# Kernel optimization log

Measured on AMD Instinct MI355X. Metric: run time of the kernel, lower is better.

The kernel has to match this reference:

```python
import jax, jax.numpy as jnp
import numpy as np

K, N, M, D, H = 3, 16384, 4096, 128, 64


def _phi(x, W1, b1, W2, b2, W3, b3):
    # x: [n, D]; weights stacked over kernels: W1 [K,H,D], W2/W3 [K,H,H], b* [K,H]
    h1 = jax.nn.softplus(jnp.einsum('nd,khd->knh', x, W1) + b1[:, None, :])
    h2 = jax.nn.softplus(jnp.einsum('knh,kgh->kng', h1, W2) + b2[:, None, :])
    return jnp.einsum('kng,kfg->knf', h2, W3) + b3[:, None, :]  # [K, n, H]


def setup_inputs() -> dict:
    key = jax.random.key(0)
    ks = jax.random.split(key, 10)
    s = lambda shp, fan: jax.random.normal(ks[0], shp)  # placeholder
    inp = {
        'x': jax.random.normal(ks[0], (N, D), jnp.float32),
        'z': jax.random.normal(ks[1], (M, D), jnp.float32),
        'W1': jax.random.normal(ks[2], (K, H, D), jnp.float32) / np.sqrt(H),
        'b1': jax.random.normal(ks[3], (K, H), jnp.float32) / np.sqrt(H),
        'W2': jax.random.normal(ks[4], (K, H, H), jnp.float32) / np.sqrt(H),
        'b2': jax.random.normal(ks[5], (K, H), jnp.float32) / np.sqrt(H),
        'W3': jax.random.normal(ks[6], (K, H, H), jnp.float32) / np.sqrt(H),
        'b3': jax.random.normal(ks[7], (K, H), jnp.float32) / np.sqrt(H),
        'log_sigma': jnp.array([0.0, 0.5185, 1.0], jnp.float32),
        'kernel_weights': jnp.zeros((K,), jnp.float32),
    }
    return inp


def reference(x, z, W1, b1, W2, b2, W3, b3, log_sigma, kernel_weights):
    fx = _phi(x, W1, b1, W2, b2, W3, b3)  # [K, N, H]
    fz = _phi(z, W1, b1, W2, b2, W3, b3)  # [K, M, H]
    # pairwise squared distance via expansion (same math as ((fx-fz)**2).sum(-1))
    sq = (jnp.sum(fx * fx, -1)[:, :, None]
          + jnp.sum(fz * fz, -1)[:, None, :]
          - 2.0 * jnp.einsum('knh,kmh->knm', fx, fz))  # [K, N, M]
    sq = jnp.maximum(sq, 0.0)
    inv2sig = 1.0 / (2.0 * jnp.power(10.0, log_sigma))  # [K]
    kxz = jnp.exp(-inv2sig[:, None, None] * sq)  # [K, N, M]
    w = jax.nn.softmax(kernel_weights)  # [K]
    return jnp.einsum('k,knm->nm', w, kxz)  # [N, M]
```

## Files before the change

### kernel.cpp

```cpp
#include <hip/hip_runtime.h>

typedef _Float16 half8 __attribute__((ext_vector_type(8)));
typedef float floatx4 __attribute__((ext_vector_type(4)));

#define K_ 3
#define N_ 16384
#define M_ 4096
#define D_ 128
#define H_ 64

#define OFF_FXH 0
#define SZ_FXH (K_*N_*H_*2)
#define OFF_FZH (OFF_FXH + SZ_FXH)
#define SZ_FZH (K_*M_*H_*2)
#define OFF_NXS (OFF_FZH + SZ_FZH)
#define SZ_NXS (K_*N_*4)
#define OFF_NZS (OFF_NXS + SZ_NXS)
#define SZ_NZS (K_*M_*4)
#define OFF_W1T (OFF_NZS + SZ_NZS)
#define SZ_W1T (K_*D_*H_*4)
#define OFF_W2T (OFF_W1T + SZ_W1T)
#define SZ_W2T (K_*H_*H_*4)
#define OFF_W3T (OFF_W2T + SZ_W2T)

__global__ void transpose_w(const float* __restrict__ W1,
                            const float* __restrict__ W2,
                            const float* __restrict__ W3,
                            float* __restrict__ W1t,
                            float* __restrict__ W2t,
                            float* __restrict__ W3t) {
  int idx = blockIdx.x * 256 + threadIdx.x;
  if (idx < K_*H_*D_) {
    int k = idx / (H_*D_); int r = idx % (H_*D_);
    int h = r / D_; int d = r % D_;
    W1t[k*(D_*H_) + d*H_ + h] = W1[idx];
  }
  if (idx < K_*H_*H_) {
    int k = idx / (H_*H_); int r = idx % (H_*H_);
    int g = r / H_; int h = r % H_;
    W2t[k*(H_*H_) + h*H_ + g] = W2[idx];
    W3t[k*(H_*H_) + h*H_ + g] = W3[idx];
  }
}

__device__ __forceinline__ float softplus_f(float x) {
  float p = exp2f(x * 1.44269504089f);
  float r = 0.693147180560f * log2f(1.0f + p);
  return (x > 20.0f) ? x : r;
}

__global__ __launch_bounds__(256) void phi_kernel(
    const float* __restrict__ x, const float* __restrict__ z,
    const float* __restrict__ W1t, const float* __restrict__ b1,
    const float* __restrict__ W2t, const float* __restrict__ b2,
    const float* __restrict__ W3t, const float* __restrict__ b3,
    const float* __restrict__ log_sigma,
    _Float16* __restrict__ fxh, float* __restrict__ nxs,
    _Float16* __restrict__ fzh, float* __restrict__ nzs)
{
  __shared__ float hbuf[64*68];
  __shared__ float nred[64*4];

  const int which = blockIdx.z;
  const int nrows = which ? M_ : N_;
  if (blockIdx.x * 64 >= nrows) return;
  const float* __restrict__ src = which ? z : x;
  _Float16* __restrict__ dsth = which ? fzh : fxh;
  float* __restrict__ dstn = which ? nzs : nxs;

  const int t = threadIdx.x;
  const int lane = t & 63;
  const int wv = __builtin_amdgcn_readfirstlane(t >> 6);
  const int k = blockIdx.y;
  const int row = blockIdx.x * 64 + lane;
  const int h0 = wv * 16;

  const float* __restrict__ w1 = W1t + k*(D_*H_);
  const float* __restrict__ w2 = W2t + k*(H_*H_);
  const float* __restrict__ w3 = W3t + k*(H_*H_);

  float acc[16];
  #pragma unroll
  for (int i=0;i<16;i++) acc[i] = b1[k*H_ + h0 + i];
  const float4* __restrict__ xr = (const float4*)(src + (size_t)row * D_);
  #pragma unroll 2
  for (int d4=0; d4<D_/4; d4++) {
    float4 xv = xr[d4];
    const float* wd = w1 + d4*4*H_ + h0;
    #pragma unroll
    for (int i=0;i<16;i++) acc[i] = fmaf(xv.x, wd[i], acc[i]);
    #pragma unroll
    for (int i=0;i<16;i++) acc[i] = fmaf(xv.y, wd[H_+i], acc[i]);
    #pragma unroll
    for (int i=0;i<16;i++) acc[i] = fmaf(xv.z, wd[2*H_+i], acc[i]);
    #pragma unroll
    for (int i=0;i<16;i++) acc[i] = fmaf(xv.w, wd[3*H_+i], acc[i]);
  }
  #pragma unroll
  for (int i=0;i<16;i+=4) {
    float4 v;
    v.x = softplus_f(acc[i+0]); v.y = softplus_f(acc[i+1]);
    v.z = softplus_f(acc[i+2]); v.w = softplus_f(acc[i+3]);
    *(float4*)&hbuf[lane*68 + h0 + i] = v;
  }
  __syncthreads();
  #pragma unroll
  for (int i=0;i<16;i++) acc[i] = b2[k*H_ + h0 + i];
  #pragma unroll 2
  for (int h4=0; h4<H_/4; h4++) {
    float4 hv = *(const float4*)&hbuf[lane*68 + h4*4];
    const float* wd = w2 + h4*4*H_ + h0;
    #pragma unroll
    for (int i=0;i<16;i++) acc[i] = fmaf(hv.x, wd[i], acc[i]);
    #pragma unroll
    for (int i=0;i<16;i++) acc[i] = fmaf(hv.y, wd[H_+i], acc[i]);
    #pragma unroll
    for (int i=0;i<16;i++) acc[i] = fmaf(hv.z, wd[2*H_+i], acc[i]);
    #pragma unroll
    for (int i=0;i<16;i++) acc[i] = fmaf(hv.w, wd[3*H_+i], acc[i]);
  }
  __syncthreads();
  #pragma unroll
  for (int i=0;i<16;i+=4) {
    float4 v;
    v.x = softplus_f(acc[i+0]); v.y = softplus_f(acc[i+1]);
    v.z = softplus_f(acc[i+2]); v.w = softplus_f(acc[i+3]);
    *(float4*)&hbuf[lane*68 + h0 + i] = v;
  }
  __syncthreads();
  #pragma unroll
  for (int i=0;i<16;i++) acc[i] = b3[k*H_ + h0 + i];
  #pragma unroll 2
  for (int h4=0; h4<H_/4; h4++) {
    float4 hv = *(const float4*)&hbuf[lane*68 + h4*4];
    const float* wd = w3 + h4*4*H_ + h0;
    #pragma unroll
    for (int i=0;i<16;i++) acc[i] = fmaf(hv.x, wd[i], acc[i]);
    #pragma unroll
    for (int i=0;i<16;i++) acc[i] = fmaf(hv.y, wd[H_+i], acc[i]);
    #pragma unroll
    for (int i=0;i<16;i++) acc[i] = fmaf(hv.z, wd[2*H_+i], acc[i]);
    #pragma unroll
    for (int i=0;i<16;i++) acc[i] = fmaf(hv.w, wd[3*H_+i], acc[i]);
  }
  float lsv = log_sigma[k];
  float inv2sig = 0.5f * exp2f(-lsv * 3.32192809489f);
  float c2 = inv2sig * 1.44269504089f;
  float s = sqrtf(c2);
  half8 u0, u1;
  float nsum = 0.f;
  #pragma unroll
  for (int i=0;i<8;i++) {
    _Float16 v = (_Float16)(s * acc[i]);
    u0[i] = v; float f = (float)v; nsum = fmaf(f, f, nsum);
  }
  #pragma unroll
  for (int i=0;i<8;i++) {
    _Float16 v = (_Float16)(s * acc[8+i]);
    u1[i] = v; float f = (float)v; nsum = fmaf(f, f, nsum);
  }
  _Float16* dp = dsth + ((size_t)k*nrows + row)*H_ + h0;
  *(half8*)dp = u0;
  *(half8*)(dp + 8) = u1;
  nred[lane*4 + wv] = nsum;
  __syncthreads();
  if (t < 64) {
    float v = nred[t*4+0] + nred[t*4+1] + nred[t*4+2] + nred[t*4+3];
    dstn[(size_t)k*nrows + row] = v;
  }
}

__global__ __launch_bounds__(256, 2) void dkef_main(
    const _Float16* __restrict__ fxh, const _Float16* __restrict__ fzh,
    const float* __restrict__ nxs, const float* __restrict__ nzs,
    const float* __restrict__ kw, float* __restrict__ out)
{
  __shared__ __align__(16) _Float16 Ab[128*72];
  __shared__ __align__(16) _Float16 Bb[128*72];
  __shared__ float nxl[128];
  __shared__ float nzl[128];

  const int t = threadIdx.x;
  const int lane = t & 63;
  const int wv = t >> 6;
  const int m0 = blockIdx.x * 128;
  const int n0 = blockIdx.y * 128;

  float k0 = kw[0], k1 = kw[1], k2 = kw[2];
  float mx = fmaxf(k0, fmaxf(k1, k2));
  float e0 = exp2f((k0 - mx) * 1.44269504089f);
  float e1 = exp2f((k1 - mx) * 1.44269504089f);
  float e2 = exp2f((k2 - mx) * 1.44269504089f);
  float winv = 1.0f / (e0 + e1 + e2);
  float wk3[3] = {e0 * winv, e1 * winv, e2 * winv};

  const int wa = (wv >> 1) * 64;
  const int wb = (wv & 1) * 64;
  const int fr = lane & 15;
  const int fq = lane >> 4;

  floatx4 oacc[4][4] = {};

  for (int k = 0; k < K_; k++) {
    __syncthreads();
    {
      const int4* ga = (const int4*)(fxh + ((size_t)k*N_ + n0)*H_);
      #pragma unroll
      for (int it = 0; it < 4; it++) {
        int idx = t + it*256;
        int r = idx >> 3, c = idx & 7;
        *(int4*)&Ab[r*72 + c*8] = ga[idx];
      }
      const int4* gb = (const int4*)(fzh + ((size_t)k*M_ + m0)*H_);
      #pragma unroll
      for (int it = 0; it < 4; it++) {
        int idx = t + it*256;
        int r = idx >> 3, c = idx & 7;
        *(int4*)&Bb[r*72 + c*8] = gb[idx];
      }
      if (t < 128) nxl[t] = nxs[(size_t)k*N_ + n0 + t];
      else         nzl[t-128] = nzs[(size_t)k*M_ + m0 + (t-128)];
    }
    __syncthreads();

    floatx4 dacc[4][4] = {};
    #pragma unroll
    for (int ks = 0; ks < 2; ks++) {
      half8 af[4], bf[4];
      #pragma unroll
      for (int i = 0; i < 4; i++)
        af[i] = *(const half8*)&Ab[(wa + i*16 + fr)*72 + ks*32 + fq*8];
      #pragma unroll
      for (int j = 0; j < 4; j++)
        bf[j] = *(const half8*)&Bb[(wb + j*16 + fr)*72 + ks*32 + fq*8];
      #pragma unroll
      for (int i = 0; i < 4; i++)
        #pragma unroll
        for (int j = 0; j < 4; j++)
          dacc[i][j] = __builtin_amdgcn_mfma_f32_16x16x32_f16(af[i], bf[j], dacc[i][j], 0, 0, 0);
    }

    float wkv = wk3[k];
    #pragma unroll
    for (int i = 0; i < 4; i++) {
      floatx4 nx4 = *(const floatx4*)&nxl[wa + i*16 + fq*4];
      #pragma unroll
      for (int j = 0; j < 4; j++) {
        float nzv = nzl[wb + j*16 + fr];
        #pragma unroll
        for (int r = 0; r < 4; r++) {
          float sm = nx4[r] + nzv;
          float e = fmaf(2.0f, dacc[i][j][r], -sm);
          e = fminf(e, 0.0f);
          oacc[i][j][r] = fmaf(wkv, exp2f(e), oacc[i][j][r]);
        }
      }
    }
  }

  #pragma unroll
  for (int i = 0; i < 4; i++) {
    #pragma unroll
    for (int r = 0; r < 4; r++) {
      size_t rowg = (size_t)(n0 + wa + i*16 + fq*4 + r);
      float* orow = out + rowg * M_ + m0 + wb + fr;
      #pragma unroll
      for (int j = 0; j < 4; j++) orow[j*16] = oacc[i][j][r];
    }
  }
}

extern "C" void kernel_launch(void* const* d_in, const int* in_sizes, int n_in,
                              void* d_out, int out_size, void* d_ws, size_t ws_size,
                              hipStream_t stream) {
  const float* x  = (const float*)d_in[0];
  const float* z  = (const float*)d_in[1];
  const float* W1 = (const float*)d_in[2];
  const float* b1 = (const float*)d_in[3];
  const float* W2 = (const float*)d_in[4];
  const float* b2 = (const float*)d_in[5];
  const float* W3 = (const float*)d_in[6];
  const float* b3 = (const float*)d_in[7];
  const float* ls = (const float*)d_in[8];
  const float* kw = (const float*)d_in[9];
  float* out = (float*)d_out;

  char* ws = (char*)d_ws;
  _Float16* fxh = (_Float16*)(ws + OFF_FXH);
  _Float16* fzh = (_Float16*)(ws + OFF_FZH);
  float* nxs = (float*)(ws + OFF_NXS);
  float* nzs = (float*)(ws + OFF_NZS);
  float* W1t = (float*)(ws + OFF_W1T);
  float* W2t = (float*)(ws + OFF_W2T);
  float* W3t = (float*)(ws + OFF_W3T);

  hipLaunchKernelGGL(transpose_w, dim3((K_*H_*D_ + 255)/256), dim3(256), 0, stream,
                     W1, W2, W3, W1t, W2t, W3t);
  hipLaunchKernelGGL(phi_kernel, dim3(N_/64, K_, 2), dim3(256), 0, stream,
                     x, z, W1t, b1, W2t, b2, W3t, b3, ls, fxh, nxs, fzh, nzs);
  hipLaunchKernelGGL(dkef_main, dim3(M_/128, N_/128), dim3(256), 0, stream,
                     fxh, fzh, nxs, nzs, kw, out);
}
```

Baseline: 383.7 us.

## Stage phi inputs in swizzled LDS, widen phi blocks, split dkef accumulators

The phi kernel now runs 512 threads per block, so each wave computes 8 hidden units instead of 16. The input rows are staged into XOR-swizzled shared memory with coalesced loads, replacing strided per-thread global reads, and the hidden buffer uses a swizzle in place of padding. The main kernel computes its distance MFMA tile in two halves to cut live accumulator registers, and raises the launch-bounds occupancy hint from 2 to 3 blocks. The trade-offs are more LDS per phi block and extra operand reloads for the split tile.

New measurement: 412.7 us. 1.08x slower.

```diff
diff --git a/kernel.cpp b/kernel.cpp
--- a/kernel.cpp
+++ b/kernel.cpp
@@ -49,7 +49,7 @@
   return (x > 20.0f) ? x : r;
 }
 
-__global__ __launch_bounds__(256) void phi_kernel(
+__global__ __launch_bounds__(512) void phi_kernel(
     const float* __restrict__ x, const float* __restrict__ z,
     const float* __restrict__ W1t, const float* __restrict__ b1,
     const float* __restrict__ W2t, const float* __restrict__ b2,
@@ -58,8 +58,9 @@
     _Float16* __restrict__ fxh, float* __restrict__ nxs,
     _Float16* __restrict__ fzh, float* __restrict__ nzs)
 {
-  __shared__ float hbuf[64*68];
-  __shared__ float nred[64*4];
+  __shared__ float xbuf[64*128];
+  __shared__ float hbuf[64*64];
+  __shared__ float nred[64*8];
 
   const int which = blockIdx.z;
   const int nrows = which ? M_ : N_;
@@ -69,108 +70,120 @@
   float* __restrict__ dstn = which ? nzs : nxs;
 
   const int t = threadIdx.x;
-  const int lane = t & 63;
+  const int row = t & 63;
   const int wv = __builtin_amdgcn_readfirstlane(t >> 6);
   const int k = blockIdx.y;
-  const int row = blockIdx.x * 64 + lane;
-  const int h0 = wv * 16;
+  const int rowg = blockIdx.x * 64 + row;
+  const int h0 = wv * 8;
 
   const float* __restrict__ w1 = W1t + k*(D_*H_);
   const float* __restrict__ w2 = W2t + k*(H_*H_);
   const float* __restrict__ w3 = W3t + k*(H_*H_);
 
-  float acc[16];
-  #pragma unroll
-  for (int i=0;i<16;i++) acc[i] = b1[k*H_ + h0 + i];
-  const float4* __restrict__ xr = (const float4*)(src + (size_t)row * D_);
+  {
+    const float4* gx = (const float4*)src + (size_t)(blockIdx.x * 64) * 32;
+    #pragma unroll
+    for (int it = 0; it < 4; it++) {
+      int gidx = t + it*512;
+      float4 v = gx[gidx];
+      int r = gidx >> 5, c = gidx & 31;
+      *(float4*)&xbuf[r*128 + (((c ^ (r & 31)) << 2))] = v;
+    }
+  }
+  __syncthreads();
+
+  float acc[8];
+  #pragma unroll
+  for (int i=0;i<8;i++) acc[i] = b1[k*H_ + h0 + i];
   #pragma unroll 2
   for (int d4=0; d4<D_/4; d4++) {
-    float4 xv = xr[d4];
+    float4 xv = *(const float4*)&xbuf[row*128 + ((d4 ^ (row & 31)) << 2)];
     const float* wd = w1 + d4*4*H_ + h0;
     #pragma unroll
-    for (int i=0;i<16;i++) acc[i] = fmaf(xv.x, wd[i], acc[i]);
-    #pragma unroll
-    for (int i=0;i<16;i++) acc[i] = fmaf(xv.y, wd[H_+i], acc[i]);
-    #pragma unroll
-    for (int i=0;i<16;i++) acc[i] = fmaf(xv.z, wd[2*H_+i], acc[i]);
-    #pragma unroll
-    for (int i=0;i<16;i++) acc[i] = fmaf(xv.w, wd[3*H_+i], acc[i]);
-  }
-  #pragma unroll
-  for (int i=0;i<16;i+=4) {
-    float4 v;
-    v.x = softplus_f(acc[i+0]); v.y = softplus_f(acc[i+1]);
-    v.z = softplus_f(acc[i+2]); v.w = softplus_f(acc[i+3]);
-    *(float4*)&hbuf[lane*68 + h0 + i] = v;
-  }
-  __syncthreads();
-  #pragma unroll
-  for (int i=0;i<16;i++) acc[i] = b2[k*H_ + h0 + i];
+    for (int i=0;i<8;i++) acc[i] = fmaf(xv.x, wd[i], acc[i]);
+    #pragma unroll
+    for (int i=0;i<8;i++) acc[i] = fmaf(xv.y, wd[H_+i], acc[i]);
+    #pragma unroll
+    for (int i=0;i<8;i++) acc[i] = fmaf(xv.z, wd[2*H_+i], acc[i]);
+    #pragma unroll
+    for (int i=0;i<8;i++) acc[i] = fmaf(xv.w, wd[3*H_+i], acc[i]);
+  }
+  {
+    int c0 = wv*2;
+    float4 v0, v1;
+    v0.x = softplus_f(acc[0]); v0.y = softplus_f(acc[1]);
+    v0.z = softplus_f(acc[2]); v0.w = softplus_f(acc[3]);
+    v1.x = softplus_f(acc[4]); v1.y = softplus_f(acc[5]);
+    v1.z = softplus_f(acc[6]); v1.w = softplus_f(acc[7]);
+    *(float4*)&hbuf[row*64 + ((c0 ^ (row & 15)) << 2)] = v0;
+    *(float4*)&hbuf[row*64 + (((c0+1) ^ (row & 15)) << 2)] = v1;
+  }
+  __syncthreads();
+  #pragma unroll
+  for (int i=0;i<8;i++) acc[i] = b2[k*H_ + h0 + i];
   #pragma unroll 2
   for (int h4=0; h4<H_/4; h4++) {
-    float4 hv = *(const float4*)&hbuf[lane*68 + h4*4];
+    float4 hv = *(const float4*)&hbuf[row*64 + ((h4 ^ (row & 15)) << 2)];
     const float* wd = w2 + h4*4*H_ + h0;
     #pragma unroll
-    for (int i=0;i<16;i++) acc[i] = fmaf(hv.x, wd[i], acc[i]);
-    #pragma unroll
-    for (int i=0;i<16;i++) acc[i] = fmaf(hv.y, wd[H_+i], acc[i]);
-    #pragma unroll
-    for (int i=0;i<16;i++) acc[i] = fmaf(hv.z, wd[2*H_+i], acc[i]);
-    #pragma unroll
-    for (int i=0;i<16;i++) acc[i] = fmaf(hv.w, wd[3*H_+i], acc[i]);
-  }
-  __syncthreads();
-  #pragma unroll
-  for (int i=0;i<16;i+=4) {
-    float4 v;
-    v.x = softplus_f(acc[i+0]); v.y = softplus_f(acc[i+1]);
-    v.z = softplus_f(acc[i+2]); v.w = softplus_f(acc[i+3]);
-    *(float4*)&hbuf[lane*68 + h0 + i] = v;
-  }
-  __syncthreads();
-  #pragma unroll
-  for (int i=0;i<16;i++) acc[i] = b3[k*H_ + h0 + i];
+    for (int i=0;i<8;i++) acc[i] = fmaf(hv.x, wd[i], acc[i]);
+    #pragma unroll
+    for (int i=0;i<8;i++) acc[i] = fmaf(hv.y, wd[H_+i], acc[i]);
+    #pragma unroll
+    for (int i=0;i<8;i++) acc[i] = fmaf(hv.z, wd[2*H_+i], acc[i]);
+    #pragma unroll
+    for (int i=0;i<8;i++) acc[i] = fmaf(hv.w, wd[3*H_+i], acc[i]);
+  }
+  __syncthreads();
+  {
+    int c0 = wv*2;
+    float4 v0, v1;
+    v0.x = softplus_f(acc[0]); v0.y = softplus_f(acc[1]);
+    v0.z = softplus_f(acc[2]); v0.w = softplus_f(acc[3]);
+    v1.x = softplus_f(acc[4]); v1.y = softplus_f(acc[5]);
+    v1.z = softplus_f(acc[6]); v1.w = softplus_f(acc[7]);
+    *(float4*)&hbuf[row*64 + ((c0 ^ (row & 15)) << 2)] = v0;
+    *(float4*)&hbuf[row*64 + (((c0+1) ^ (row & 15)) << 2)] = v1;
+  }
+  __syncthreads();
+  #pragma unroll
+  for (int i=0;i<8;i++) acc[i] = b3[k*H_ + h0 + i];
   #pragma unroll 2
   for (int h4=0; h4<H_/4; h4++) {
-    float4 hv = *(const float4*)&hbuf[lane*68 + h4*4];
+    float4 hv = *(const float4*)&hbuf[row*64 + ((h4 ^ (row & 15)) << 2)];
     const float* wd = w3 + h4*4*H_ + h0;
     #pragma unroll
-    for (int i=0;i<16;i++) acc[i] = fmaf(hv.x, wd[i], acc[i]);
-    #pragma unroll
-    for (int i=0;i<16;i++) acc[i] = fmaf(hv.y, wd[H_+i], acc[i]);
-    #pragma unroll
-    for (int i=0;i<16;i++) acc[i] = fmaf(hv.z, wd[2*H_+i], acc[i]);
-    #pragma unroll
-    for (int i=0;i<16;i++) acc[i] = fmaf(hv.w, wd[3*H_+i], acc[i]);
+    for (int i=0;i<8;i++) acc[i] = fmaf(hv.x, wd[i], acc[i]);
+    #pragma unroll
+    for (int i=0;i<8;i++) acc[i] = fmaf(hv.y, wd[H_+i], acc[i]);
+    #pragma unroll
+    for (int i=0;i<8;i++) acc[i] = fmaf(hv.z, wd[2*H_+i], acc[i]);
+    #pragma unroll
+    for (int i=0;i<8;i++) acc[i] = fmaf(hv.w, wd[3*H_+i], acc[i]);
   }
   float lsv = log_sigma[k];
   float inv2sig = 0.5f * exp2f(-lsv * 3.32192809489f);
   float c2 = inv2sig * 1.44269504089f;
   float s = sqrtf(c2);
-  half8 u0, u1;
+  half8 u;
   float nsum = 0.f;
   #pragma unroll
   for (int i=0;i<8;i++) {
     _Float16 v = (_Float16)(s * acc[i]);
-    u0[i] = v; float f = (float)v; nsum = fmaf(f, f, nsum);
-  }
-  #pragma unroll
-  for (int i=0;i<8;i++) {
-    _Float16 v = (_Float16)(s * acc[8+i]);
-    u1[i] = v; float f = (float)v; nsum = fmaf(f, f, nsum);
-  }
-  _Float16* dp = dsth + ((size_t)k*nrows + row)*H_ + h0;
-  *(half8*)dp = u0;
-  *(half8*)(dp + 8) = u1;
-  nred[lane*4 + wv] = nsum;
+    u[i] = v; float f = (float)v; nsum = fmaf(f, f, nsum);
+  }
+  *(half8*)(dsth + ((size_t)k*nrows + rowg)*H_ + h0) = u;
+  nred[row*8 + wv] = nsum;
   __syncthreads();
   if (t < 64) {
-    float v = nred[t*4+0] + nred[t*4+1] + nred[t*4+2] + nred[t*4+3];
-    dstn[(size_t)k*nrows + row] = v;
-  }
-}
-
-__global__ __launch_bounds__(256, 2) void dkef_main(
+    float v = 0.f;
+    #pragma unroll
+    for (int j=0;j<8;j++) v += nred[t*8 + j];
+    dstn[(size_t)k*nrows + blockIdx.x*64 + t] = v;
+  }
+}
+
+__global__ __launch_bounds__(256, 3) void dkef_main(
     const _Float16* __restrict__ fxh, const _Float16* __restrict__ fzh,
     const float* __restrict__ nxs, const float* __restrict__ nzs,
     const float* __restrict__ kw, float* __restrict__ out)
@@ -223,36 +236,38 @@
     }
     __syncthreads();
 
-    floatx4 dacc[4][4] = {};
-    #pragma unroll
-    for (int ks = 0; ks < 2; ks++) {
-      half8 af[4], bf[4];
-      #pragma unroll
-      for (int i = 0; i < 4; i++)
-        af[i] = *(const half8*)&Ab[(wa + i*16 + fr)*72 + ks*32 + fq*8];
-      #pragma unroll
-      for (int j = 0; j < 4; j++)
-        bf[j] = *(const half8*)&Bb[(wb + j*16 + fr)*72 + ks*32 + fq*8];
-      #pragma unroll
-      for (int i = 0; i < 4; i++)
+    float wkv = wk3[k];
+    #pragma unroll
+    for (int h = 0; h < 2; h++) {
+      floatx4 dacc[2][4] = {};
+      #pragma unroll
+      for (int ks = 0; ks < 2; ks++) {
+        half8 af[2], bf[4];
+        #pragma unroll
+        for (int i = 0; i < 2; i++)
+          af[i] = *(const half8*)&Ab[(wa + (h*2+i)*16 + fr)*72 + ks*32 + fq*8];
         #pragma unroll
         for (int j = 0; j < 4; j++)
-          dacc[i][j] = __builtin_amdgcn_mfma_f32_16x16x32_f16(af[i], bf[j], dacc[i][j], 0, 0, 0);
-    }
-
-    float wkv = wk3[k];
-    #pragma unroll
-    for (int i = 0; i < 4; i++) {
-      floatx4 nx4 = *(const floatx4*)&nxl[wa + i*16 + fq*4];
-      #pragma unroll
-      for (int j = 0; j < 4; j++) {
-        float nzv = nzl[wb + j*16 + fr];
+          bf[j] = *(const half8*)&Bb[(wb + j*16 + fr)*72 + ks*32 + fq*8];
         #pragma unroll
-        for (int r = 0; r < 4; r++) {
-          float sm = nx4[r] + nzv;
-          float e = fmaf(2.0f, dacc[i][j][r], -sm);
-          e = fminf(e, 0.0f);
-          oacc[i][j][r] = fmaf(wkv, exp2f(e), oacc[i][j][r]);
+        for (int i = 0; i < 2; i++)
+          #pragma unroll
+          for (int j = 0; j < 4; j++)
+            dacc[i][j] = __builtin_amdgcn_mfma_f32_16x16x32_f16(af[i], bf[j], dacc[i][j], 0, 0, 0);
+      }
+      #pragma unroll
+      for (int i = 0; i < 2; i++) {
+        floatx4 nx4 = *(const floatx4*)&nxl[wa + (h*2+i)*16 + fq*4];
+        #pragma unroll
+        for (int j = 0; j < 4; j++) {
+          float nzv = nzl[wb + j*16 + fr];
+          #pragma unroll
+          for (int r = 0; r < 4; r++) {
+            float sm = nx4[r] + nzv;
+            float e = fmaf(2.0f, dacc[i][j][r], -sm);
+            e = fminf(e, 0.0f);
+            oacc[h*2+i][j][r] = fmaf(wkv, exp2f(e), oacc[h*2+i][j][r]);
+          }
         }
       }
     }
@@ -296,7 +311,7 @@
 
   hipLaunchKernelGGL(transpose_w, dim3((K_*H_*D_ + 255)/256), dim3(256), 0, stream,
                      W1, W2, W3, W1t, W2t, W3t);
-  hipLaunchKernelGGL(phi_kernel, dim3(N_/64, K_, 2), dim3(256), 0, stream,
+  hipLaunchKernelGGL(phi_kernel, dim3(N_/64, K_, 2), dim3(512), 0, stream,
                      x, z, W1t, b1, W2t, b2, W3t, b3, ls, fxh, nxs, fzh, nzs);
   hipLaunchKernelGGL(dkef_main, dim3(M_/128, N_/128), dim3(256), 0, stream,
                      fxh, fzh, nxs, nzs, kw, out);
```
